# Optimization experiments

Hardware: AMD Instinct MI355X
Metric: run time of the kernel (lower is better)

## Reference

```python
import jax, jax.numpy as jnp
import numpy as np

N, D, E = 50000, 128, 800000
EPS = 1e-5


def setup_inputs() -> dict:
    key = jax.random.key(0)
    ks = jax.random.split(key, 16)
    x = jax.random.normal(ks[0], (N, D), dtype=jnp.float32)
    edge_index = jax.random.randint(ks[1], (2, E), 0, N, dtype=jnp.int32)
    s = 1.0 / np.sqrt(D)
    inp = {"x": x, "edge_index": edge_index}
    for i in range(3):
        inp[f"lng{i}"] = jnp.ones((D,), jnp.float32)
        inp[f"lnb{i}"] = jnp.zeros((D,), jnp.float32)
        inp[f"W{i}"] = jax.random.normal(ks[2 + 2 * i], (D, D), jnp.float32) * s
        inp[f"b{i}"] = jnp.zeros((D,), jnp.float32)
    return inp


def _gcn_norm(edge_index):
    # PyG GCNConv default: add self loops, symmetric normalization D^-1/2 (A+I) D^-1/2
    loop = jnp.arange(N, dtype=edge_index.dtype)
    src = jnp.concatenate([edge_index[0], loop])  # [E+N]
    dst = jnp.concatenate([edge_index[1], loop])
    deg = jax.ops.segment_sum(jnp.ones_like(dst, jnp.float32), dst, num_segments=N)
    dinv = jnp.where(deg > 0, jax.lax.rsqrt(jnp.maximum(deg, 1.0)), 0.0)
    norm = dinv[src] * dinv[dst]  # [E+N]
    return src, dst, norm


def _layer(h, g, bt, W, b, src, dst, norm):
    # LayerNorm -> ReLU -> GCNConv
    mu = jnp.mean(h, axis=-1, keepdims=True)
    var = jnp.mean(jnp.square(h - mu), axis=-1, keepdims=True)
    hn = (h - mu) * jax.lax.rsqrt(var + EPS) * g + bt
    hn = jax.nn.relu(hn) @ W  # [N, D]
    msg = norm[:, None] * hn[src]  # [E+N, D] gather
    return jax.ops.segment_sum(msg, dst, num_segments=N) + b


def reference(x, edge_index, lng0, lnb0, W0, b0, lng1, lnb1, W1, b1, lng2, lnb2, W2, b2):
    src, dst, norm = _gcn_norm(edge_index)
    # conv0 (GCNLayer) + residual
    x = _layer(x, lng0, lnb0, W0, b0, src, dst, norm) + x
    # conv1 (ResGCNLayer: two GCNLayers) + residual
    h = _layer(x, lng1, lnb1, W1, b1, src, dst, norm)
    h = _layer(h, lng2, lnb2, W2, b2, src, dst, norm)
    return h + x
```

## Files before the change

### kernel.cpp

```cpp
#include <hip/hip_runtime.h>

#define N_NODES 50000
#define DIM     128
#define E_EDGES 800000
#define ELLW    64

typedef __attribute__((ext_vector_type(8))) short short8;
typedef __attribute__((ext_vector_type(4))) float f32x4;

__device__ __forceinline__ float bflo(unsigned int u){ return __uint_as_float(u << 16); }
__device__ __forceinline__ float bfhi(unsigned int u){ return __uint_as_float(u & 0xFFFF0000u); }
__device__ __forceinline__ unsigned int f2bf(float f){
  unsigned int u = __float_as_uint(f);
  return (u + 0x7FFFu + ((u >> 16) & 1u)) >> 16;
}
__device__ __forceinline__ unsigned int pack2(float a, float b){
  return f2bf(a) | (f2bf(b) << 16);
}


__global__ __launch_bounds__(256) void count_kernel(const int* __restrict__ edges,
                                                    int* __restrict__ cnt,
                                                    int* __restrict__ epos){
  int e = blockIdx.x * 256 + threadIdx.x;
  if (e < E_EDGES) epos[e] = atomicAdd(&cnt[edges[E_EDGES + e]], 1);
}


__global__ __launch_bounds__(256) void prep_kernel(const int* __restrict__ edges,
                                                   const int* __restrict__ epos,
                                                   const int* __restrict__ cnt,
                                                   int2* __restrict__ ell,
                                                   const float* __restrict__ W0,
                                                   const float* __restrict__ W1,
                                                   const float* __restrict__ W2,
                                                   unsigned short* __restrict__ Wt){
  int u = blockIdx.x, tid = threadIdx.x;
  if (u < 3125){
    int e = u * 256 + tid;
    if (e < E_EDGES){
      int s = edges[e];
      int d = edges[E_EDGES + e];
      int pos = epos[e];
      if (pos < ELLW){
        float w = rsqrtf((float)(cnt[s] + 1)) * rsqrtf((float)(cnt[d] + 1));
        int2 pk; pk.x = s; pk.y = __float_as_int(w);
        ell[(size_t)d * ELLW + pos] = pk;
      }
    }
  } else if (u < 3125 + 196){
    int i = (u - 3125) * 256 + tid;
    if (i < N_NODES){
      int deg = cnt[i];
      int g4 = i & ~3;
      int J = max(max(cnt[g4], cnt[g4 + 1]), max(cnt[g4 + 2], cnt[g4 + 3]));
      int J4 = min(ELLW, (J + 3) & ~3);
      int2 z; z.x = 0; z.y = 0;
      for (int pp = min(deg, J4); pp < J4; ++pp)
        ell[(size_t)i * ELLW + pp] = z;
    }
  } else {
    int idx = (u - 3321) * 256 + tid;
    int w = idx >> 14, r = idx & 16383;
    const float* W = (w == 0) ? W0 : (w == 1) ? W1 : W2;
    Wt[w * 16384 + (r & 127) * 128 + (r >> 7)] = (unsigned short)f2bf(W[r]);
  }
}


__global__ __launch_bounds__(256) void gemm_ln_mfma(const float* __restrict__ X,
                                                    const float* __restrict__ g,
                                                    const float* __restrict__ bt,
                                                    const unsigned short* __restrict__ Wt,
                                                    unsigned short* __restrict__ Y){
  __shared__ unsigned short ldsb[128 * 136];
  int tid = threadIdx.x;
  #pragma unroll
  for (int it = 0; it < 8; ++it){
    int c  = tid + it * 256;
    int n  = c >> 4, kc = c & 15;
    *(short8*)&ldsb[n * 136 + kc * 8] = *(const short8*)(Wt + n * 128 + kc * 8);
  }
  int wave = tid >> 6, lane = tid & 63, quad = lane >> 4, l15 = lane & 15;
  int rowbase = blockIdx.x * 128 + wave * 32;
  int rm0 = rowbase + l15;      if (rm0 > N_NODES - 1) rm0 = N_NODES - 1;
  int rm1 = rowbase + 16 + l15; if (rm1 > N_NODES - 1) rm1 = N_NODES - 1;

  float v0[4][8], v1[4][8];
  float s0 = 0.f, ss0 = 0.f, s1 = 0.f, ss1 = 0.f;
  #pragma unroll
  for (int kk = 0; kk < 4; ++kk){
    float4 xa = *(const float4*)(X + (size_t)rm0 * 128 + kk * 32 + quad * 8);
    float4 xb = *(const float4*)(X + (size_t)rm0 * 128 + kk * 32 + quad * 8 + 4);
    float4 ya = *(const float4*)(X + (size_t)rm1 * 128 + kk * 32 + quad * 8);
    float4 yb_ = *(const float4*)(X + (size_t)rm1 * 128 + kk * 32 + quad * 8 + 4);
    v0[kk][0]=xa.x; v0[kk][1]=xa.y; v0[kk][2]=xa.z; v0[kk][3]=xa.w;
    v0[kk][4]=xb.x; v0[kk][5]=xb.y; v0[kk][6]=xb.z; v0[kk][7]=xb.w;
    v1[kk][0]=ya.x; v1[kk][1]=ya.y; v1[kk][2]=ya.z; v1[kk][3]=ya.w;
    v1[kk][4]=yb_.x; v1[kk][5]=yb_.y; v1[kk][6]=yb_.z; v1[kk][7]=yb_.w;
    #pragma unroll
    for (int j = 0; j < 8; ++j){
      s0 += v0[kk][j]; ss0 += v0[kk][j] * v0[kk][j];
      s1 += v1[kk][j]; ss1 += v1[kk][j] * v1[kk][j];
    }
  }
  s0 += __shfl_xor(s0, 16, 64); ss0 += __shfl_xor(ss0, 16, 64);
  s0 += __shfl_xor(s0, 32, 64); ss0 += __shfl_xor(ss0, 32, 64);
  s1 += __shfl_xor(s1, 16, 64); ss1 += __shfl_xor(ss1, 16, 64);
  s1 += __shfl_xor(s1, 32, 64); ss1 += __shfl_xor(ss1, 32, 64);
  float mu0 = s0 * (1.0f/128.0f), var0 = ss0 * (1.0f/128.0f) - mu0*mu0;
  float mu1 = s1 * (1.0f/128.0f), var1 = ss1 * (1.0f/128.0f) - mu1*mu1;
  float rs0 = rsqrtf(var0 + 1e-5f), rs1 = rsqrtf(var1 + 1e-5f);

  short8 a0[4], a1[4];
  #pragma unroll
  for (int kk = 0; kk < 4; ++kk){
    float4 ga = *(const float4*)(g  + kk * 32 + quad * 8);
    float4 gb = *(const float4*)(g  + kk * 32 + quad * 8 + 4);
    float4 ba = *(const float4*)(bt + kk * 32 + quad * 8);
    float4 bb = *(const float4*)(bt + kk * 32 + quad * 8 + 4);
    float gg[8] = {ga.x,ga.y,ga.z,ga.w,gb.x,gb.y,gb.z,gb.w};
    float bbv[8] = {ba.x,ba.y,ba.z,ba.w,bb.x,bb.y,bb.z,bb.w};
    #pragma unroll
    for (int j = 0; j < 8; ++j){
      float h0 = fmaxf((v0[kk][j] - mu0) * rs0 * gg[j] + bbv[j], 0.0f);
      float h1 = fmaxf((v1[kk][j] - mu1) * rs1 * gg[j] + bbv[j], 0.0f);
      a0[kk][j] = (short)f2bf(h0);
      a1[kk][j] = (short)f2bf(h1);
    }
  }

  f32x4 acc[2][8];
  #pragma unroll
  for (int mt = 0; mt < 2; ++mt)
    #pragma unroll
    for (int nt = 0; nt < 8; ++nt) acc[mt][nt] = (f32x4){0.f, 0.f, 0.f, 0.f};
  __syncthreads();
  #pragma unroll
  for (int kk = 0; kk < 4; ++kk){
    #pragma unroll
    for (int nt = 0; nt < 8; ++nt){
      short8 b = *(const short8*)&ldsb[(nt * 16 + l15) * 136 + kk * 32 + quad * 8];
      acc[0][nt] = __builtin_amdgcn_mfma_f32_16x16x32_bf16(a0[kk], b, acc[0][nt], 0, 0, 0);
      acc[1][nt] = __builtin_amdgcn_mfma_f32_16x16x32_bf16(a1[kk], b, acc[1][nt], 0, 0, 0);
    }
  }
  #pragma unroll
  for (int mt = 0; mt < 2; ++mt)
    #pragma unroll
    for (int nt = 0; nt < 8; ++nt)
      #pragma unroll
      for (int r = 0; r < 4; ++r){
        int row = rowbase + mt * 16 + quad * 4 + r;
        if (row < N_NODES)
          Y[(size_t)row * 128 + nt * 16 + l15] = (unsigned short)f2bf(acc[mt][nt][r]);
      }
}


__global__ __launch_bounds__(256) void gemm_mfma(const unsigned short* __restrict__ A,
                                                 const unsigned short* __restrict__ Wt,
                                                 unsigned short* __restrict__ Y){
  __shared__ unsigned short ldsb[128 * 136];
  int tid = threadIdx.x;
  #pragma unroll
  for (int it = 0; it < 8; ++it){
    int c  = tid + it * 256;
    int n  = c >> 4, kc = c & 15;
    *(short8*)&ldsb[n * 136 + kc * 8] = *(const short8*)(Wt + n * 128 + kc * 8);
  }
  int wave = tid >> 6, lane = tid & 63, quad = lane >> 4, l15 = lane & 15;
  int rowbase = blockIdx.x * 128 + wave * 32;
  int rm0 = rowbase + l15;      if (rm0 > N_NODES - 1) rm0 = N_NODES - 1;
  int rm1 = rowbase + 16 + l15; if (rm1 > N_NODES - 1) rm1 = N_NODES - 1;

  short8 a0[4], a1[4];
  #pragma unroll
  for (int kk = 0; kk < 4; ++kk){
    a0[kk] = *(const short8*)(A + (size_t)rm0 * 128 + kk * 32 + quad * 8);
    a1[kk] = *(const short8*)(A + (size_t)rm1 * 128 + kk * 32 + quad * 8);
  }
  f32x4 acc[2][8];
  #pragma unroll
  for (int mt = 0; mt < 2; ++mt)
    #pragma unroll
    for (int nt = 0; nt < 8; ++nt) acc[mt][nt] = (f32x4){0.f, 0.f, 0.f, 0.f};
  __syncthreads();
  #pragma unroll
  for (int kk = 0; kk < 4; ++kk){
    #pragma unroll
    for (int nt = 0; nt < 8; ++nt){
      short8 b = *(const short8*)&ldsb[(nt * 16 + l15) * 136 + kk * 32 + quad * 8];
      acc[0][nt] = __builtin_amdgcn_mfma_f32_16x16x32_bf16(a0[kk], b, acc[0][nt], 0, 0, 0);
      acc[1][nt] = __builtin_amdgcn_mfma_f32_16x16x32_bf16(a1[kk], b, acc[1][nt], 0, 0, 0);
    }
  }
  #pragma unroll
  for (int mt = 0; mt < 2; ++mt)
    #pragma unroll
    for (int nt = 0; nt < 8; ++nt)
      #pragma unroll
      for (int r = 0; r < 4; ++r){
        int row = rowbase + mt * 16 + quad * 4 + r;
        if (row < N_NODES)
          Y[(size_t)row * 128 + nt * 16 + l15] = (unsigned short)f2bf(acc[mt][nt][r]);
      }
}


template<bool HAS_RES, bool DO_LN>
__global__ __launch_bounds__(256) void agg_kernel(const unsigned short* __restrict__ y,
                                                  const int* __restrict__ cnt,
                                                  const int2* __restrict__ ell,
                                                  const float* __restrict__ bias,
                                                  const float* __restrict__ res,
                                                  float* __restrict__ outp,
                                                  const float* __restrict__ lng,
                                                  const float* __restrict__ lnb,
                                                  unsigned short* __restrict__ hn_out){
  int wv   = (blockIdx.x * 256 + threadIdx.x) >> 6;
  int lane = threadIdx.x & 63;
  int hl   = lane & 15;
  int node = wv * 4 + (lane >> 4);
  int selbase = lane & 48;
  const uint4* y4 = (const uint4*)y;

  int deg = cnt[node];
  float di = rsqrtf((float)(deg + 1));
  float ws = di * di;

  const int2* row = ell + (size_t)node * ELLW;
  int2 e0 = row[hl], e1 = row[hl + 16], e2 = row[hl + 32], e3 = row[hl + 48];

  int J = deg;
  J = max(J, __shfl_xor(J, 16, 64));
  J = max(J, __shfl_xor(J, 32, 64));

  uint4 us = y4[(size_t)node * 16 + hl];
  float acc0 = ws * bflo(us.x), acc1 = ws * bfhi(us.x);
  float acc2 = ws * bflo(us.y), acc3 = ws * bfhi(us.y);
  float acc4 = ws * bflo(us.z), acc5 = ws * bfhi(us.z);
  float acc6 = ws * bflo(us.w), acc7 = ws * bfhi(us.w);

  auto block16 = [&](int2 ee, int base16){
    int rem = J - base16;
    if (rem <= 0) return;
    int nch = (min(rem, 16) + 3) >> 2;
    for (int c = 0; c < nch; ++c){
      int rb = c * 4;
      int sA = __shfl(ee.x, selbase | (rb + 0), 64);
      int sB = __shfl(ee.x, selbase | (rb + 1), 64);
      int sC = __shfl(ee.x, selbase | (rb + 2), 64);
      int sD = __shfl(ee.x, selbase | (rb + 3), 64);
      float wA = __uint_as_float((unsigned)__shfl(ee.y, selbase | (rb + 0), 64));
      float wB = __uint_as_float((unsigned)__shfl(ee.y, selbase | (rb + 1), 64));
      float wC = __uint_as_float((unsigned)__shfl(ee.y, selbase | (rb + 2), 64));
      float wD = __uint_as_float((unsigned)__shfl(ee.y, selbase | (rb + 3), 64));
      uint4 gA = y4[(size_t)sA * 16 + hl];
      uint4 gB = y4[(size_t)sB * 16 + hl];
      uint4 gC = y4[(size_t)sC * 16 + hl];
      uint4 gD = y4[(size_t)sD * 16 + hl];
      acc0 += wA*bflo(gA.x); acc1 += wA*bfhi(gA.x); acc2 += wA*bflo(gA.y); acc3 += wA*bfhi(gA.y);
      acc4 += wA*bflo(gA.z); acc5 += wA*bfhi(gA.z); acc6 += wA*bflo(gA.w); acc7 += wA*bfhi(gA.w);
      acc0 += wB*bflo(gB.x); acc1 += wB*bfhi(gB.x); acc2 += wB*bflo(gB.y); acc3 += wB*bfhi(gB.y);
      acc4 += wB*bflo(gB.z); acc5 += wB*bfhi(gB.z); acc6 += wB*bflo(gB.w); acc7 += wB*bfhi(gB.w);
      acc0 += wC*bflo(gC.x); acc1 += wC*bfhi(gC.x); acc2 += wC*bflo(gC.y); acc3 += wC*bfhi(gC.y);
      acc4 += wC*bflo(gC.z); acc5 += wC*bfhi(gC.z); acc6 += wC*bflo(gC.w); acc7 += wC*bfhi(gC.w);
      acc0 += wD*bflo(gD.x); acc1 += wD*bfhi(gD.x); acc2 += wD*bflo(gD.y); acc3 += wD*bfhi(gD.y);
      acc4 += wD*bflo(gD.z); acc5 += wD*bfhi(gD.z); acc6 += wD*bflo(gD.w); acc7 += wD*bfhi(gD.w);
    }
  };
  block16(e0, 0); block16(e1, 16); block16(e2, 32); block16(e3, 48);

  float4 ubA = ((const float4*)bias)[hl * 2];
  float4 ubB = ((const float4*)bias)[hl * 2 + 1];
  acc0 += ubA.x; acc1 += ubA.y; acc2 += ubA.z; acc3 += ubA.w;
  acc4 += ubB.x; acc5 += ubB.y; acc6 += ubB.z; acc7 += ubB.w;
  if (HAS_RES){
    float4 urA = ((const float4*)res)[(size_t)node * 32 + hl * 2];
    float4 urB = ((const float4*)res)[(size_t)node * 32 + hl * 2 + 1];
    acc0 += urA.x; acc1 += urA.y; acc2 += urA.z; acc3 += urA.w;
    acc4 += urB.x; acc5 += urB.y; acc6 += urB.z; acc7 += urB.w;
  }
  if (outp){
    float4 oA; oA.x = acc0; oA.y = acc1; oA.z = acc2; oA.w = acc3;
    float4 oB; oB.x = acc4; oB.y = acc5; oB.z = acc6; oB.w = acc7;
    ((float4*)outp)[(size_t)node * 32 + hl * 2]     = oA;
    ((float4*)outp)[(size_t)node * 32 + hl * 2 + 1] = oB;
  }

  if (DO_LN){
    float s  = acc0 + acc1 + acc2 + acc3 + acc4 + acc5 + acc6 + acc7;
    float ss = acc0*acc0 + acc1*acc1 + acc2*acc2 + acc3*acc3
             + acc4*acc4 + acc5*acc5 + acc6*acc6 + acc7*acc7;
    #pragma unroll
    for (int d = 8; d >= 1; d >>= 1){ s += __shfl_xor(s, d, 64); ss += __shfl_xor(ss, d, 64); }
    float mu  = s * (1.0f / 128.0f);
    float var = ss * (1.0f / 128.0f) - mu * mu;
    float rs  = rsqrtf(var + 1e-5f);
    float4 ugA = ((const float4*)lng)[hl * 2];
    float4 ugB = ((const float4*)lng)[hl * 2 + 1];
    float4 ubbA = ((const float4*)lnb)[hl * 2];
    float4 ubbB = ((const float4*)lnb)[hl * 2 + 1];
    float h0 = fmaxf((acc0 - mu) * rs * ugA.x + ubbA.x, 0.0f);
    float h1 = fmaxf((acc1 - mu) * rs * ugA.y + ubbA.y, 0.0f);
    float h2 = fmaxf((acc2 - mu) * rs * ugA.z + ubbA.z, 0.0f);
    float h3 = fmaxf((acc3 - mu) * rs * ugA.w + ubbA.w, 0.0f);
    float h4 = fmaxf((acc4 - mu) * rs * ugB.x + ubbB.x, 0.0f);
    float h5 = fmaxf((acc5 - mu) * rs * ugB.y + ubbB.y, 0.0f);
    float h6 = fmaxf((acc6 - mu) * rs * ugB.z + ubbB.z, 0.0f);
    float h7 = fmaxf((acc7 - mu) * rs * ugB.w + ubbB.w, 0.0f);
    uint4 ho;
    ho.x = pack2(h0, h1); ho.y = pack2(h2, h3);
    ho.z = pack2(h4, h5); ho.w = pack2(h6, h7);
    ((uint4*)hn_out)[(size_t)node * 16 + hl] = ho;
  }
}


extern "C" void kernel_launch(void* const* d_in, const int* in_sizes, int n_in,
                              void* d_out, int out_size, void* d_ws, size_t ws_size,
                              hipStream_t stream){
  const float* x    = (const float*)d_in[0];
  const int*   edges= (const int*)d_in[1];
  const float* lng0 = (const float*)d_in[2];
  const float* lnb0 = (const float*)d_in[3];
  const float* W0   = (const float*)d_in[4];
  const float* b0   = (const float*)d_in[5];
  const float* lng1 = (const float*)d_in[6];
  const float* lnb1 = (const float*)d_in[7];
  const float* W1   = (const float*)d_in[8];
  const float* b1   = (const float*)d_in[9];
  const float* lng2 = (const float*)d_in[10];
  const float* lnb2 = (const float*)d_in[11];
  const float* W2   = (const float*)d_in[12];
  const float* b2   = (const float*)d_in[13];

  char* p = (char*)d_ws;
  auto carve = [&](size_t bytes) -> void* {
    void* r = (void*)p;
    p += (bytes + 255) & ~(size_t)255;
    return r;
  };
  int*   cnt   = (int*)  carve(N_NODES * 4);
  int*   epos  = (int*)  carve((size_t)E_EDGES * 4);
  int2*  ell   = (int2*) carve((size_t)N_NODES * ELLW * 8);
  unsigned short* Wt = (unsigned short*)carve(3 * 128 * 128 * 2);
  unsigned short* hn = (unsigned short*)carve((size_t)N_NODES * 128 * 2);
  unsigned short* yb = (unsigned short*)carve((size_t)N_NODES * 128 * 2);
  float* out = (float*)d_out;

  hipMemsetAsync(cnt, 0, N_NODES * 4, stream);

  count_kernel<<<(E_EDGES + 255) / 256, 256, 0, stream>>>(edges, cnt, epos);
  prep_kernel<<<3513, 256, 0, stream>>>(edges, epos, cnt, ell, W0, W1, W2, Wt);

  const int GEMM_GRID = (N_NODES + 127) / 128;
  const int AGG_GRID  = N_NODES / 4 / 4;

  gemm_ln_mfma<<<GEMM_GRID, 256, 0, stream>>>(x, lng0, lnb0, Wt, yb);
  agg_kernel<true, true><<<AGG_GRID, 256, 0, stream>>>(yb, cnt, ell,
                                                       b0, x, out, lng1, lnb1, hn);
  gemm_mfma<<<GEMM_GRID, 256, 0, stream>>>(hn, Wt + 16384, yb);
  agg_kernel<false, true><<<AGG_GRID, 256, 0, stream>>>(yb, cnt, ell,
                                                        b1, nullptr, nullptr, lng2, lnb2, hn);
  gemm_mfma<<<GEMM_GRID, 256, 0, stream>>>(hn, Wt + 32768, yb);
  agg_kernel<true, false><<<AGG_GRID, 256, 0, stream>>>(yb, cnt, ell,
                                                        b2, out, out, nullptr, nullptr, nullptr);
}
```

Before: 295.0 us.

## Split aggregation across feature slices and move LayerNorm back into GEMM

The aggregation kernel now gives each node 8 lanes instead of 16 and splits the 128 features into four 32-wide slices, one per block, so a gather loads 8 bytes per lane and blocks are narrower and more numerous. The fused LayerNorm/ReLU epilogue leaves aggregation, since a slice cannot see the full row. Layers 1 and 2 instead use the LN-fused GEMM, reading fp32 activations from out or from a new fp32 buffer h2p. The ELL zero padding is widened to groups of 8 nodes to match the 8-node wave grouping. The cost is extra fp32 traffic between stages and neighbor index lists re-read for each of the four slices.

```diff
diff --git a/kernel.cpp b/kernel.cpp
--- a/kernel.cpp
+++ b/kernel.cpp
@@ -13,9 +13,6 @@
 __device__ __forceinline__ unsigned int f2bf(float f){
   unsigned int u = __float_as_uint(f);
   return (u + 0x7FFFu + ((u >> 16) & 1u)) >> 16;
-}
-__device__ __forceinline__ unsigned int pack2(float a, float b){
-  return f2bf(a) | (f2bf(b) << 16);
 }
 
 
@@ -52,8 +49,10 @@
     int i = (u - 3125) * 256 + tid;
     if (i < N_NODES){
       int deg = cnt[i];
-      int g4 = i & ~3;
-      int J = max(max(cnt[g4], cnt[g4 + 1]), max(cnt[g4 + 2], cnt[g4 + 3]));
+      int g8 = i & ~7;
+      int J = 0;
+      #pragma unroll
+      for (int j = 0; j < 8; ++j) J = max(J, cnt[g8 + j]);
       int J4 = min(ELLW, (J + 3) & ~3);
       int2 z; z.x = 0; z.y = 0;
       for (int pp = min(deg, J4); pp < J4; ++pp)
@@ -158,162 +157,76 @@
 }
 
 
-__global__ __launch_bounds__(256) void gemm_mfma(const unsigned short* __restrict__ A,
-                                                 const unsigned short* __restrict__ Wt,
-                                                 unsigned short* __restrict__ Y){
-  __shared__ unsigned short ldsb[128 * 136];
-  int tid = threadIdx.x;
-  #pragma unroll
-  for (int it = 0; it < 8; ++it){
-    int c  = tid + it * 256;
-    int n  = c >> 4, kc = c & 15;
-    *(short8*)&ldsb[n * 136 + kc * 8] = *(const short8*)(Wt + n * 128 + kc * 8);
-  }
-  int wave = tid >> 6, lane = tid & 63, quad = lane >> 4, l15 = lane & 15;
-  int rowbase = blockIdx.x * 128 + wave * 32;
-  int rm0 = rowbase + l15;      if (rm0 > N_NODES - 1) rm0 = N_NODES - 1;
-  int rm1 = rowbase + 16 + l15; if (rm1 > N_NODES - 1) rm1 = N_NODES - 1;
-
-  short8 a0[4], a1[4];
-  #pragma unroll
-  for (int kk = 0; kk < 4; ++kk){
-    a0[kk] = *(const short8*)(A + (size_t)rm0 * 128 + kk * 32 + quad * 8);
-    a1[kk] = *(const short8*)(A + (size_t)rm1 * 128 + kk * 32 + quad * 8);
-  }
-  f32x4 acc[2][8];
-  #pragma unroll
-  for (int mt = 0; mt < 2; ++mt)
-    #pragma unroll
-    for (int nt = 0; nt < 8; ++nt) acc[mt][nt] = (f32x4){0.f, 0.f, 0.f, 0.f};
-  __syncthreads();
-  #pragma unroll
-  for (int kk = 0; kk < 4; ++kk){
-    #pragma unroll
-    for (int nt = 0; nt < 8; ++nt){
-      short8 b = *(const short8*)&ldsb[(nt * 16 + l15) * 136 + kk * 32 + quad * 8];
-      acc[0][nt] = __builtin_amdgcn_mfma_f32_16x16x32_bf16(a0[kk], b, acc[0][nt], 0, 0, 0);
-      acc[1][nt] = __builtin_amdgcn_mfma_f32_16x16x32_bf16(a1[kk], b, acc[1][nt], 0, 0, 0);
-    }
-  }
-  #pragma unroll
-  for (int mt = 0; mt < 2; ++mt)
-    #pragma unroll
-    for (int nt = 0; nt < 8; ++nt)
-      #pragma unroll
-      for (int r = 0; r < 4; ++r){
-        int row = rowbase + mt * 16 + quad * 4 + r;
-        if (row < N_NODES)
-          Y[(size_t)row * 128 + nt * 16 + l15] = (unsigned short)f2bf(acc[mt][nt][r]);
-      }
-}
-
-
-template<bool HAS_RES, bool DO_LN>
+template<bool HAS_RES>
 __global__ __launch_bounds__(256) void agg_kernel(const unsigned short* __restrict__ y,
                                                   const int* __restrict__ cnt,
                                                   const int2* __restrict__ ell,
                                                   const float* __restrict__ bias,
                                                   const float* __restrict__ res,
-                                                  float* __restrict__ outp,
-                                                  const float* __restrict__ lng,
-                                                  const float* __restrict__ lnb,
-                                                  unsigned short* __restrict__ hn_out){
-  int wv   = (blockIdx.x * 256 + threadIdx.x) >> 6;
-  int lane = threadIdx.x & 63;
-  int hl   = lane & 15;
-  int node = wv * 4 + (lane >> 4);
-  int selbase = lane & 48;
-  const uint4* y4 = (const uint4*)y;
-
-  int deg = cnt[node];
+                                                  float* __restrict__ outp){
+  int s   = blockIdx.x & 3;
+  int g   = blockIdx.x >> 2;
+  int tid = threadIdx.x, lane = tid & 63, wave = tid >> 6;
+  int hl  = lane & 7;
+  int node = g * 32 + wave * 8 + (lane >> 3);
+  bool valid = node < N_NODES;
+  int nc = valid ? node : (N_NODES - 1);
+
+  int deg = cnt[nc];
   float di = rsqrtf((float)(deg + 1));
   float ws = di * di;
 
-  const int2* row = ell + (size_t)node * ELLW;
-  int2 e0 = row[hl], e1 = row[hl + 16], e2 = row[hl + 32], e3 = row[hl + 48];
-
-  int J = deg;
+  const int2* row = ell + (size_t)nc * ELLW;
+  int2 e0 = row[hl],      e1 = row[hl + 8],  e2 = row[hl + 16], e3 = row[hl + 24];
+  int2 e4 = row[hl + 32], e5 = row[hl + 40], e6 = row[hl + 48], e7 = row[hl + 56];
+
+  int J = valid ? deg : 0;
+  J = max(J, __shfl_xor(J, 8, 64));
   J = max(J, __shfl_xor(J, 16, 64));
   J = max(J, __shfl_xor(J, 32, 64));
 
-  uint4 us = y4[(size_t)node * 16 + hl];
-  float acc0 = ws * bflo(us.x), acc1 = ws * bfhi(us.x);
-  float acc2 = ws * bflo(us.y), acc3 = ws * bfhi(us.y);
-  float acc4 = ws * bflo(us.z), acc5 = ws * bfhi(us.z);
-  float acc6 = ws * bflo(us.w), acc7 = ws * bfhi(us.w);
-
-  auto block16 = [&](int2 ee, int base16){
-    int rem = J - base16;
+  const uint2* y2 = (const uint2*)y;
+  size_t sb = (size_t)s * 8 + hl;
+  uint2 us = y2[(size_t)nc * 32 + sb];
+  float a0 = ws * bflo(us.x), a1 = ws * bfhi(us.x);
+  float a2 = ws * bflo(us.y), a3 = ws * bfhi(us.y);
+
+  int selbase = lane & 56;
+  auto block8 = [&](int2 ee, int base8){
+    int rem = J - base8;
     if (rem <= 0) return;
-    int nch = (min(rem, 16) + 3) >> 2;
-    for (int c = 0; c < nch; ++c){
-      int rb = c * 4;
-      int sA = __shfl(ee.x, selbase | (rb + 0), 64);
-      int sB = __shfl(ee.x, selbase | (rb + 1), 64);
-      int sC = __shfl(ee.x, selbase | (rb + 2), 64);
-      int sD = __shfl(ee.x, selbase | (rb + 3), 64);
-      float wA = __uint_as_float((unsigned)__shfl(ee.y, selbase | (rb + 0), 64));
-      float wB = __uint_as_float((unsigned)__shfl(ee.y, selbase | (rb + 1), 64));
-      float wC = __uint_as_float((unsigned)__shfl(ee.y, selbase | (rb + 2), 64));
-      float wD = __uint_as_float((unsigned)__shfl(ee.y, selbase | (rb + 3), 64));
-      uint4 gA = y4[(size_t)sA * 16 + hl];
-      uint4 gB = y4[(size_t)sB * 16 + hl];
-      uint4 gC = y4[(size_t)sC * 16 + hl];
-      uint4 gD = y4[(size_t)sD * 16 + hl];
-      acc0 += wA*bflo(gA.x); acc1 += wA*bfhi(gA.x); acc2 += wA*bflo(gA.y); acc3 += wA*bfhi(gA.y);
-      acc4 += wA*bflo(gA.z); acc5 += wA*bfhi(gA.z); acc6 += wA*bflo(gA.w); acc7 += wA*bfhi(gA.w);
-      acc0 += wB*bflo(gB.x); acc1 += wB*bfhi(gB.x); acc2 += wB*bflo(gB.y); acc3 += wB*bfhi(gB.y);
-      acc4 += wB*bflo(gB.z); acc5 += wB*bfhi(gB.z); acc6 += wB*bflo(gB.w); acc7 += wB*bfhi(gB.w);
-      acc0 += wC*bflo(gC.x); acc1 += wC*bfhi(gC.x); acc2 += wC*bflo(gC.y); acc3 += wC*bfhi(gC.y);
-      acc4 += wC*bflo(gC.z); acc5 += wC*bfhi(gC.z); acc6 += wC*bflo(gC.w); acc7 += wC*bfhi(gC.w);
-      acc0 += wD*bflo(gD.x); acc1 += wD*bfhi(gD.x); acc2 += wD*bflo(gD.y); acc3 += wD*bfhi(gD.y);
-      acc4 += wD*bflo(gD.z); acc5 += wD*bfhi(gD.z); acc6 += wD*bflo(gD.w); acc7 += wD*bfhi(gD.w);
+    int jn = (min(rem, 8) + 3) & ~3;
+    for (int j = 0; j < jn; j += 4){
+      int sA = __shfl(ee.x, selbase | (j + 0), 64);
+      int sB = __shfl(ee.x, selbase | (j + 1), 64);
+      int sC = __shfl(ee.x, selbase | (j + 2), 64);
+      int sD = __shfl(ee.x, selbase | (j + 3), 64);
+      float wA = __uint_as_float((unsigned)__shfl(ee.y, selbase | (j + 0), 64));
+      float wB = __uint_as_float((unsigned)__shfl(ee.y, selbase | (j + 1), 64));
+      float wC = __uint_as_float((unsigned)__shfl(ee.y, selbase | (j + 2), 64));
+      float wD = __uint_as_float((unsigned)__shfl(ee.y, selbase | (j + 3), 64));
+      uint2 gA = y2[(size_t)sA * 32 + sb];
+      uint2 gB = y2[(size_t)sB * 32 + sb];
+      uint2 gC = y2[(size_t)sC * 32 + sb];
+      uint2 gD = y2[(size_t)sD * 32 + sb];
+      a0 += wA*bflo(gA.x); a1 += wA*bfhi(gA.x); a2 += wA*bflo(gA.y); a3 += wA*bfhi(gA.y);
+      a0 += wB*bflo(gB.x); a1 += wB*bfhi(gB.x); a2 += wB*bflo(gB.y); a3 += wB*bfhi(gB.y);
+      a0 += wC*bflo(gC.x); a1 += wC*bfhi(gC.x); a2 += wC*bflo(gC.y); a3 += wC*bfhi(gC.y);
+      a0 += wD*bflo(gD.x); a1 += wD*bfhi(gD.x); a2 += wD*bflo(gD.y); a3 += wD*bfhi(gD.y);
     }
   };
-  block16(e0, 0); block16(e1, 16); block16(e2, 32); block16(e3, 48);
-
-  float4 ubA = ((const float4*)bias)[hl * 2];
-  float4 ubB = ((const float4*)bias)[hl * 2 + 1];
-  acc0 += ubA.x; acc1 += ubA.y; acc2 += ubA.z; acc3 += ubA.w;
-  acc4 += ubB.x; acc5 += ubB.y; acc6 += ubB.z; acc7 += ubB.w;
+  block8(e0, 0);  block8(e1, 8);  block8(e2, 16); block8(e3, 24);
+  block8(e4, 32); block8(e5, 40); block8(e6, 48); block8(e7, 56);
+
+  float4 ub = ((const float4*)bias)[sb];
+  a0 += ub.x; a1 += ub.y; a2 += ub.z; a3 += ub.w;
   if (HAS_RES){
-    float4 urA = ((const float4*)res)[(size_t)node * 32 + hl * 2];
-    float4 urB = ((const float4*)res)[(size_t)node * 32 + hl * 2 + 1];
-    acc0 += urA.x; acc1 += urA.y; acc2 += urA.z; acc3 += urA.w;
-    acc4 += urB.x; acc5 += urB.y; acc6 += urB.z; acc7 += urB.w;
-  }
-  if (outp){
-    float4 oA; oA.x = acc0; oA.y = acc1; oA.z = acc2; oA.w = acc3;
-    float4 oB; oB.x = acc4; oB.y = acc5; oB.z = acc6; oB.w = acc7;
-    ((float4*)outp)[(size_t)node * 32 + hl * 2]     = oA;
-    ((float4*)outp)[(size_t)node * 32 + hl * 2 + 1] = oB;
-  }
-
-  if (DO_LN){
-    float s  = acc0 + acc1 + acc2 + acc3 + acc4 + acc5 + acc6 + acc7;
-    float ss = acc0*acc0 + acc1*acc1 + acc2*acc2 + acc3*acc3
-             + acc4*acc4 + acc5*acc5 + acc6*acc6 + acc7*acc7;
-    #pragma unroll
-    for (int d = 8; d >= 1; d >>= 1){ s += __shfl_xor(s, d, 64); ss += __shfl_xor(ss, d, 64); }
-    float mu  = s * (1.0f / 128.0f);
-    float var = ss * (1.0f / 128.0f) - mu * mu;
-    float rs  = rsqrtf(var + 1e-5f);
-    float4 ugA = ((const float4*)lng)[hl * 2];
-    float4 ugB = ((const float4*)lng)[hl * 2 + 1];
-    float4 ubbA = ((const float4*)lnb)[hl * 2];
-    float4 ubbB = ((const float4*)lnb)[hl * 2 + 1];
-    float h0 = fmaxf((acc0 - mu) * rs * ugA.x + ubbA.x, 0.0f);
-    float h1 = fmaxf((acc1 - mu) * rs * ugA.y + ubbA.y, 0.0f);
-    float h2 = fmaxf((acc2 - mu) * rs * ugA.z + ubbA.z, 0.0f);
-    float h3 = fmaxf((acc3 - mu) * rs * ugA.w + ubbA.w, 0.0f);
-    float h4 = fmaxf((acc4 - mu) * rs * ugB.x + ubbB.x, 0.0f);
-    float h5 = fmaxf((acc5 - mu) * rs * ugB.y + ubbB.y, 0.0f);
-    float h6 = fmaxf((acc6 - mu) * rs * ugB.z + ubbB.z, 0.0f);
-    float h7 = fmaxf((acc7 - mu) * rs * ugB.w + ubbB.w, 0.0f);
-    uint4 ho;
-    ho.x = pack2(h0, h1); ho.y = pack2(h2, h3);
-    ho.z = pack2(h4, h5); ho.w = pack2(h6, h7);
-    ((uint4*)hn_out)[(size_t)node * 16 + hl] = ho;
+    float4 ur = ((const float4*)res)[(size_t)nc * 32 + sb];
+    a0 += ur.x; a1 += ur.y; a2 += ur.z; a3 += ur.w;
+  }
+  if (valid){
+    float4 o; o.x = a0; o.y = a1; o.z = a2; o.w = a3;
+    ((float4*)outp)[(size_t)node * 32 + sb] = o;
   }
 }
 
@@ -345,9 +258,9 @@
   int*   cnt   = (int*)  carve(N_NODES * 4);
   int*   epos  = (int*)  carve((size_t)E_EDGES * 4);
   int2*  ell   = (int2*) carve((size_t)N_NODES * ELLW * 8);
-  unsigned short* Wt = (unsigned short*)carve(3 * 128 * 128 * 2);
-  unsigned short* hn = (unsigned short*)carve((size_t)N_NODES * 128 * 2);
-  unsigned short* yb = (unsigned short*)carve((size_t)N_NODES * 128 * 2);
+  unsigned short* Wt  = (unsigned short*)carve(3 * 128 * 128 * 2);
+  unsigned short* yb  = (unsigned short*)carve((size_t)N_NODES * 128 * 2);
+  float*          h2p = (float*)carve((size_t)N_NODES * 128 * 4);
   float* out = (float*)d_out;
 
   hipMemsetAsync(cnt, 0, N_NODES * 4, stream);
@@ -356,15 +269,12 @@
   prep_kernel<<<3513, 256, 0, stream>>>(edges, epos, cnt, ell, W0, W1, W2, Wt);
 
   const int GEMM_GRID = (N_NODES + 127) / 128;
-  const int AGG_GRID  = N_NODES / 4 / 4;
+  const int AGG_GRID  = ((N_NODES + 31) / 32) * 4;
 
   gemm_ln_mfma<<<GEMM_GRID, 256, 0, stream>>>(x, lng0, lnb0, Wt, yb);
-  agg_kernel<true, true><<<AGG_GRID, 256, 0, stream>>>(yb, cnt, ell,
-                                                       b0, x, out, lng1, lnb1, hn);
-  gemm_mfma<<<GEMM_GRID, 256, 0, stream>>>(hn, Wt + 16384, yb);
-  agg_kernel<false, true><<<AGG_GRID, 256, 0, stream>>>(yb, cnt, ell,
-                                                        b1, nullptr, nullptr, lng2, lnb2, hn);
-  gemm_mfma<<<GEMM_GRID, 256, 0, stream>>>(hn, Wt + 32768, yb);
-  agg_kernel<true, false><<<AGG_GRID, 256, 0, stream>>>(yb, cnt, ell,
-                                                        b2, out, out, nullptr, nullptr, nullptr);
-}
+  agg_kernel<true><<<AGG_GRID, 256, 0, stream>>>(yb, cnt, ell, b0, x, out);
+  gemm_ln_mfma<<<GEMM_GRID, 256, 0, stream>>>(out, lng1, lnb1, Wt + 16384, yb);
+  agg_kernel<false><<<AGG_GRID, 256, 0, stream>>>(yb, cnt, ell, b1, nullptr, h2p);
+  gemm_ln_mfma<<<GEMM_GRID, 256, 0, stream>>>(h2p, lng2, lnb2, Wt + 32768, yb);
+  agg_kernel<true><<<AGG_GRID, 256, 0, stream>>>(yb, cnt, ell, b2, out, out);
+}
```

Result: slower. 355.4 us (+20.5%).
